# Kernel optimization log

Hardware: AMD Instinct MI355X
Metric: run time of the kernel (lower is better)

Reference implementation:

```python
import jax, jax.numpy as jnp
import numpy as np
from math import sqrt

N_HEADS = 16

def setup_inputs() -> dict:
    key = jax.random.key(0)
    ks = jax.random.split(key, 6)
    B, T, C = 4, 2048, 1024
    s = 0.02
    return {
        "X": jax.random.normal(ks[0], (B, T, C), jnp.float32),
        "Wq": jax.random.normal(ks[1], (C, C), jnp.float32) * s,
        "Wk": jax.random.normal(ks[2], (C, C), jnp.float32) * s,
        "Wv": jax.random.normal(ks[3], (C, C), jnp.float32) * s,
        "Wo": jax.random.normal(ks[4], (C, C), jnp.float32) * s,
        "bo": jnp.zeros((C,), jnp.float32),
    }

def reference(X, Wq, Wk, Wv, Wo, bo):
    B, T, C = X.shape
    H = N_HEADS
    D = C // H
    scale = sqrt(C / H)  # == sqrt(D)
    # Linear layers (torch Linear: y = x @ W.T), split into heads: [B,H,T,D]
    Q = (X @ Wq.T).reshape(B, T, H, D).transpose(0, 2, 1, 3)
    K = (X @ Wk.T).reshape(B, T, H, D).transpose(0, 2, 1, 3)
    V = (X @ Wv.T).reshape(B, T, H, D).transpose(0, 2, 1, 3)
    A = jnp.einsum("bhtd,bhsd->bhts", Q, K) / scale  # [B,H,T,T]
    causal = jnp.tril(jnp.ones((T, T), dtype=bool))
    A = jnp.where(causal, A, -jnp.inf)
    A = jax.nn.softmax(A, axis=-1)
    Y = jnp.einsum("bhts,bhsd->bhtd", A, V)  # [B,H,T,D]
    Y = Y.transpose(0, 2, 1, 3).reshape(B, T, C)
    return Y @ Wo.T + bo
```

## Files before the change

kernel.cpp:

```cpp
#include <hip/hip_runtime.h>
#include <hip/hip_bf16.h>
#include <stdint.h>


typedef unsigned short u16;
typedef __attribute__((ext_vector_type(8))) __bf16 bf16x8;
typedef __attribute__((ext_vector_type(4))) float  f32x4;
typedef __attribute__((ext_vector_type(4))) unsigned short u16x4;
typedef __attribute__((ext_vector_type(4))) short s16x4;

#define B_  4
#define T_  2048
#define C_  1024
#define H_  16
#define D_  64
#define BT_ (B_ * T_)

#define Q_SCALE 0.1803368801111204f

__device__ __forceinline__ u16 f32_to_bf16(float f) {
    unsigned int u = __float_as_uint(f);
    unsigned int r = (u + 0x7FFFu + ((u >> 16) & 1u)) >> 16;
    return (u16)r;
}

__device__ __forceinline__ unsigned int pk_bf16(float a, float b) {
    float2 f2; f2.x = a; f2.y = b;
    __hip_bfloat162 h = __float22bfloat162_rn(f2);
    return *(unsigned int*)&h;
}

__device__ __forceinline__ void async16(const void* g, void* lds) {
    __builtin_amdgcn_global_load_lds(
        (const __attribute__((address_space(1))) void*)g,
        (__attribute__((address_space(3))) void*)lds, 16, 0, 0);
}

__global__ void cast_bf16_kernel(const float* __restrict__ in, u16* __restrict__ out, int n4) {
    int i = blockIdx.x * 256 + threadIdx.x;
    if (i >= n4) return;
    float4 v = ((const float4*)in)[i];
    u16x4 o;
    o[0] = f32_to_bf16(v.x); o[1] = f32_to_bf16(v.y);
    o[2] = f32_to_bf16(v.z); o[3] = f32_to_bf16(v.w);
    ((u16x4*)out)[i] = o;
}

__global__ void cast_w4_kernel(const float* __restrict__ w0, const float* __restrict__ w1,
                               const float* __restrict__ w2, const float* __restrict__ w3,
                               u16* __restrict__ o0, u16* __restrict__ o1,
                               u16* __restrict__ o2, u16* __restrict__ o3) {
    int which = blockIdx.y;
    const float* in = (which == 0) ? w0 : (which == 1) ? w1 : (which == 2) ? w2 : w3;
    u16* out = (which == 0) ? o0 : (which == 1) ? o1 : (which == 2) ? o2 : o3;
    int i = blockIdx.x * 256 + threadIdx.x;
    float4 v = ((const float4*)in)[i];
    u16x4 o;
    o[0] = f32_to_bf16(v.x); o[1] = f32_to_bf16(v.y);
    o[2] = f32_to_bf16(v.z); o[3] = f32_to_bf16(v.w);
    ((u16x4*)out)[i] = o;
}

__device__ __forceinline__ void gemm_core_128_db(
    const u16* __restrict__ A, const u16* __restrict__ B,
    u16* As, u16* Bs, int m0, int n0, f32x4 (&acc)[4][4])
{
    const int K = C_;
    const int KT = K / 32;
    int tid  = threadIdx.x;
    int lane = tid & 63, w = tid >> 6;
    int quad = lane >> 4, l15 = lane & 15;
    int wm = w >> 1, wn = w & 1;

    int c0 = tid, c1 = tid + 256;
    int row0 = c0 >> 2, row1 = c1 >> 2;
    int gc0 = (((c0 & 3) - (row0 >> 1)) & 3) * 8;
    int gc1 = (((c1 & 3) - (row1 >> 1)) & 3) * 8;
    int ldsb0 = (w * 64) * 16;
    int ldsb1 = (256 + w * 64) * 16;

    const u16* ApA = A + (size_t)(m0 + row0) * K + gc0;
    const u16* ApB = A + (size_t)(m0 + row1) * K + gc1;
    const u16* BpA = B + (size_t)(n0 + row0) * K + gc0;
    const u16* BpB = B + (size_t)(n0 + row1) * K + gc1;

    char* As0 = (char*)As; char* As1 = (char*)As + 8192;
    char* Bs0 = (char*)Bs; char* Bs1 = (char*)Bs + 8192;

    int aoff[4], boff[4];
#pragma unroll
    for (int i = 0; i < 4; ++i) {
        int rA = wm * 64 + i * 16 + l15;
        aoff[i] = (rA * 32 + (((rA >> 1) + quad) & 3) * 8) * 2;
        int rB = wn * 64 + i * 16 + l15;
        boff[i] = (rB * 32 + (((rB >> 1) + quad) & 3) * 8) * 2;
    }

    async16(ApA, As0 + ldsb0); async16(ApB, As0 + ldsb1);
    async16(BpA, Bs0 + ldsb0); async16(BpB, Bs0 + ldsb1);
    ApA += 32; ApB += 32; BpA += 32; BpB += 32;

    auto body = [&](int kt, const char* Ac, const char* Bc, char* Apf, char* Bpf) {
        __syncthreads();
        if (kt + 1 < KT) {
            async16(ApA, Apf + ldsb0); async16(ApB, Apf + ldsb1);
            async16(BpA, Bpf + ldsb0); async16(BpB, Bpf + ldsb1);
        }
        ApA += 32; ApB += 32; BpA += 32; BpB += 32;

        bf16x8 a[4], b[4];
#pragma unroll
        for (int i = 0; i < 4; ++i) {
            a[i] = *(const bf16x8*)(Ac + aoff[i]);
            b[i] = *(const bf16x8*)(Bc + boff[i]);
        }
#pragma unroll
        for (int i = 0; i < 4; ++i)
#pragma unroll
            for (int j = 0; j < 4; ++j)
                acc[i][j] = __builtin_amdgcn_mfma_f32_16x16x32_bf16(a[i], b[j], acc[i][j], 0, 0, 0);
    };

    for (int kt = 0; kt < KT; kt += 2) {
        body(kt,     As0, Bs0, As1, Bs1);
        body(kt + 1, As1, Bs1, As0, Bs0);
    }
}

__global__ __launch_bounds__(256, 4) void qkv_gemm(
    const u16* __restrict__ Xb,
    const u16* __restrict__ Wqb, const u16* __restrict__ Wkb, const u16* __restrict__ Wvb,
    u16* __restrict__ Qb, u16* __restrict__ Kb, u16* __restrict__ Vtb)
{
    __shared__ u16 As[2 * 128 * 32];
    __shared__ u16 Bs[2 * 128 * 32];

    int id = blockIdx.x;
    int xcd = id & 7;
    int local = id >> 3;
    int yloc = local & 7;
    int zx = local >> 3;
    int bx = zx & 7;
    int which = zx >> 3;
    int by = xcd * 8 + yloc;

    const u16* W = (which == 0) ? Wqb : ((which == 1) ? Wkb : Wvb);

    f32x4 acc[4][4];
    const f32x4 z4 = {0.f, 0.f, 0.f, 0.f};
#pragma unroll
    for (int i = 0; i < 4; ++i)
#pragma unroll
        for (int j = 0; j < 4; ++j) acc[i][j] = z4;

    int lane = threadIdx.x & 63, w = threadIdx.x >> 6;
    int quad = lane >> 4, l15 = lane & 15;
    int wm = w >> 1, wn = w & 1;

    if (which <= 1) {
        int m0 = bx * 128, n0 = by * 128;
        gemm_core_128_db(W, Xb, As, Bs, m0, n0, acc);
        float s = (which == 0) ? Q_SCALE : 1.0f;
        u16* Out = (which == 0) ? Qb : Kb;
#pragma unroll
        for (int i = 0; i < 4; ++i) {
            int ch0 = m0 + wm * 64 + i * 16 + quad * 4;
#pragma unroll
            for (int j = 0; j < 4; ++j) {
                int t = n0 + wn * 64 + j * 16 + l15;
                u16x4 v;
#pragma unroll
                for (int r = 0; r < 4; ++r) v[r] = f32_to_bf16(acc[i][j][r] * s);
                *(u16x4*)&Out[(size_t)t * C_ + ch0] = v;
            }
        }
    } else {
        int m0 = by * 128, n0 = bx * 128;
        gemm_core_128_db(Xb, W, As, Bs, m0, n0, acc);
#pragma unroll
        for (int i = 0; i < 4; ++i) {
            int t0 = m0 + wm * 64 + i * 16 + quad * 4;
#pragma unroll
            for (int j = 0; j < 4; ++j) {
                int col = n0 + wn * 64 + j * 16 + l15;
                int h = col >> 6, d = col & 63;
                u16x4 v;
#pragma unroll
                for (int r = 0; r < 4; ++r) v[r] = f32_to_bf16(acc[i][j][r]);
                int b = t0 >> 11, t = t0 & (T_ - 1);
                *(u16x4*)&Vtb[(((b * H_ + h) * D_ + d) * T_) + t] = v;
            }
        }
    }
}

__global__ __launch_bounds__(256) void attn_kernel(
    const u16* __restrict__ Qb, const u16* __restrict__ Kb,
    const u16* __restrict__ Vtb, u16* __restrict__ Yb)
{
    __shared__ u16 Ks0[64 * 64], Ks1[64 * 64];
    __shared__ u16 Vs0[64 * 64], Vs1[64 * 64];

    int id = blockIdx.x;
    int kk = id >> 8;
    int cc = id & 255;
    int jj = cc >> 6;
    int bh = cc & 63;
    int qt = (kk == 0) ? jj : (kk == 1) ? (15 - jj) : (kk == 2) ? (jj + 4) : (11 - jj);

    int tid = threadIdx.x, lane = tid & 63, w = tid >> 6;
    int quad = lane >> 4, l15 = lane & 15;
    int qbase = qt * 128;
    int b = bh >> 4, h = bh & 15;

    bf16x8 qf[2][2];
    {
        const u16* q0 = Qb + ((size_t)(b * T_ + qbase + w * 32 + l15)) * C_ + h * 64;
        qf[0][0] = *(const bf16x8*)(q0 + quad * 8);
        qf[0][1] = *(const bf16x8*)(q0 + 32 + quad * 8);
        const u16* q1 = q0 + 16 * C_;
        qf[1][0] = *(const bf16x8*)(q1 + quad * 8);
        qf[1][1] = *(const bf16x8*)(q1 + 32 + quad * 8);
    }

    int koff0[4], koff1[4], voff[4][4];
#pragma unroll
    for (int sblk = 0; sblk < 4; ++sblk) {
        int sr = sblk * 16 + l15;
        koff0[sblk] = (sr * 64 + ((quad + sr) & 7) * 8) * 2;
        koff1[sblk] = (sr * 64 + ((4 + quad + sr) & 7) * 8) * 2;
    }
#pragma unroll
    for (int n = 0; n < 4; ++n)
#pragma unroll
        for (int sblk = 0; sblk < 4; ++sblk) {
            int dr = n * 16 + l15;
            voff[n][sblk] = (dr * 64 + ((sblk * 2 + (quad >> 1) + dr) & 7) * 8 + (quad & 1) * 4) * 2;
        }

    float l_part[2] = {0.f, 0.f};
    f32x4 o_acc[2][4];
    const f32x4 z4 = {0.f, 0.f, 0.f, 0.f};
#pragma unroll
    for (int c = 0; c < 2; ++c)
#pragma unroll
        for (int n = 0; n < 4; ++n) o_acc[c][n] = z4;

    int cA = tid, cB = tid + 256;
    int sA = cA >> 3, sB = cB >> 3;
    int offA = (((cA & 7) - sA) & 7) * 8;
    int offB = (((cB & 7) - sB) & 7) * 8;
    const u16* Kbase = Kb + (size_t)(b * T_) * C_ + h * 64;
    const u16* Vbase = Vtb + (size_t)bh * D_ * T_;
    int ldsb0 = (w * 64) * 16, ldsb1 = (256 + w * 64) * 16;

    const int nst = 2 * qt + 2;

    const u16* kgpA = Kbase + (size_t)sA * C_ + offA;
    const u16* kgpB = Kbase + (size_t)sB * C_ + offB;
    const u16* vgpA = Vbase + sA * T_ + offA;
    const u16* vgpB = Vbase + sB * T_ + offB;

    async16(kgpA, (char*)Ks0 + ldsb0);
    async16(kgpB, (char*)Ks0 + ldsb1);
    async16(vgpA, (char*)Vs0 + ldsb0);
    async16(vgpB, (char*)Vs0 + ldsb1);
    kgpA += 64 * C_; kgpB += 64 * C_; vgpA += 64; vgpB += 64;

    auto tile_body = [&](int st, const u16* K_, const u16* V_, char* Kpf, char* Vpf) {
        __syncthreads();
        if (st + 1 < nst) {
            async16(kgpA, Kpf + ldsb0);
            async16(kgpB, Kpf + ldsb1);
            async16(vgpA, Vpf + ldsb0);
            async16(vgpB, Vpf + ldsb1);
        }
        kgpA += 64 * C_; kgpB += 64 * C_; vgpA += 64; vgpB += 64;

        f32x4 sv[2][4];
#pragma unroll
        for (int sblk = 0; sblk < 4; ++sblk) {
            bf16x8 k0 = *(const bf16x8*)((const char*)K_ + koff0[sblk]);
            bf16x8 k1 = *(const bf16x8*)((const char*)K_ + koff1[sblk]);
#pragma unroll
            for (int c = 0; c < 2; ++c) {
                f32x4 t0 = __builtin_amdgcn_mfma_f32_16x16x32_bf16(k0, qf[c][0], z4, 0, 0, 0);
                sv[c][sblk] = __builtin_amdgcn_mfma_f32_16x16x32_bf16(k1, qf[c][1], t0, 0, 0, 0);
            }
        }

        if (st >= 2 * qt) {
            int sb0 = st * 64 - qbase;
#pragma unroll
            for (int c = 0; c < 2; ++c) {
                int tl = w * 32 + c * 16 + l15;
#pragma unroll
                for (int sblk = 0; sblk < 4; ++sblk)
#pragma unroll
                    for (int r = 0; r < 4; ++r)
                        if (sb0 + sblk * 16 + quad * 4 + r > tl) sv[c][sblk][r] = -1e30f;
            }
        }

        s16x4 pfrag[2][4];
#pragma unroll
        for (int c = 0; c < 2; ++c) {
            f32x4 s4 = z4;
#pragma unroll
            for (int sblk = 0; sblk < 4; ++sblk) {
#pragma unroll
                for (int r = 0; r < 4; ++r)
                    sv[c][sblk][r] = __builtin_amdgcn_exp2f(sv[c][sblk][r]);
                s4 += sv[c][sblk];
                uint2 pk;
                pk.x = pk_bf16(sv[c][sblk][0], sv[c][sblk][1]);
                pk.y = pk_bf16(sv[c][sblk][2], sv[c][sblk][3]);
                pfrag[c][sblk] = *(s16x4*)&pk;
            }
            l_part[c] += (s4[0] + s4[1]) + (s4[2] + s4[3]);
        }

#pragma unroll
        for (int n = 0; n < 4; ++n)
#pragma unroll
            for (int sblk = 0; sblk < 4; ++sblk) {
                s16x4 va = *(const s16x4*)((const char*)V_ + voff[n][sblk]);
#pragma unroll
                for (int c = 0; c < 2; ++c)
                    o_acc[c][n] = __builtin_amdgcn_mfma_f32_16x16x16bf16_1k(va, pfrag[c][sblk], o_acc[c][n], 0, 0, 0);
            }
    };

    for (int st = 0; st < nst; st += 2) {
        tile_body(st,     Ks0, Vs0, (char*)Ks1, (char*)Vs1);
        tile_body(st + 1, Ks1, Vs1, (char*)Ks0, (char*)Vs0);
    }

#pragma unroll
    for (int c = 0; c < 2; ++c) {
        float l = l_part[c];
        l += __shfl_xor(l, 16, 64);
        l += __shfl_xor(l, 32, 64);
        float inv = 1.0f / l;
        int t = qbase + w * 32 + c * 16 + l15;
        size_t rowoff = ((size_t)b * T_ + t) * C_ + h * 64;
#pragma unroll
        for (int n = 0; n < 4; ++n) {
            uint2 pk;
            pk.x = pk_bf16(o_acc[c][n][0] * inv, o_acc[c][n][1] * inv);
            pk.y = pk_bf16(o_acc[c][n][2] * inv, o_acc[c][n][3] * inv);
            *(uint2*)&Yb[rowoff + n * 16 + quad * 4] = pk;
        }
    }
}

__global__ __launch_bounds__(256, 4) void proj_gemm(
    const u16* __restrict__ Yb, const u16* __restrict__ Wob,
    const float* __restrict__ bo, float* __restrict__ out)
{
    __shared__ u16 As[2 * 128 * 32];
    __shared__ u16 Bs[2 * 128 * 32];

    int id = blockIdx.x;
    int xcd = id & 7;
    int local = id >> 3;
    int by = xcd * 8 + (local & 7);
    int bx = local >> 3;
    int m0 = bx * 128, n0 = by * 128;

    f32x4 acc[4][4];
    const f32x4 z4 = {0.f, 0.f, 0.f, 0.f};
#pragma unroll
    for (int i = 0; i < 4; ++i)
#pragma unroll
        for (int j = 0; j < 4; ++j) acc[i][j] = z4;

    gemm_core_128_db(Wob, Yb, As, Bs, m0, n0, acc);

    int lane = threadIdx.x & 63, w = threadIdx.x >> 6;
    int quad = lane >> 4, l15 = lane & 15;
    int wm = w >> 1, wn = w & 1;

#pragma unroll
    for (int i = 0; i < 4; ++i) {
        int ch0 = m0 + wm * 64 + i * 16 + quad * 4;
        float4 b4 = *(const float4*)&bo[ch0];
#pragma unroll
        for (int j = 0; j < 4; ++j) {
            int t = n0 + wn * 64 + j * 16 + l15;
            float4 o;
            o.x = acc[i][j][0] + b4.x;
            o.y = acc[i][j][1] + b4.y;
            o.z = acc[i][j][2] + b4.z;
            o.w = acc[i][j][3] + b4.w;
            *(float4*)&out[(size_t)t * C_ + ch0] = o;
        }
    }
}

extern "C" void kernel_launch(void* const* d_in, const int* in_sizes, int n_in,
                              void* d_out, int out_size, void* d_ws, size_t ws_size,
                              hipStream_t stream) {
    const float* X  = (const float*)d_in[0];
    const float* Wq = (const float*)d_in[1];
    const float* Wk = (const float*)d_in[2];
    const float* Wv = (const float*)d_in[3];
    const float* Wo = (const float*)d_in[4];
    const float* bo = (const float*)d_in[5];

    char* ws = (char*)d_ws;
    u16* Xb  = (u16*)(ws);
    u16* Wqb = (u16*)(ws + (16u << 20));
    u16* Wkb = (u16*)(ws + (18u << 20));
    u16* Wvb = (u16*)(ws + (20u << 20));
    u16* Wob = (u16*)(ws + (22u << 20));
    u16* Qb  = (u16*)(ws + (24u << 20));
    u16* Kb  = (u16*)(ws + (40u << 20));
    u16* Vtb = (u16*)(ws + (56u << 20));
    u16* Yb  = (u16*)(ws + (72u << 20));

    cast_bf16_kernel<<<(BT_ * C_ / 4) / 256, 256, 0, stream>>>(X, Xb, BT_ * C_ / 4);
    cast_w4_kernel<<<dim3((C_ * C_ / 4) / 256, 4), 256, 0, stream>>>(
        Wq, Wk, Wv, Wo, Wqb, Wkb, Wvb, Wob);

    qkv_gemm<<<dim3(3 * 8 * 64), 256, 0, stream>>>(Xb, Wqb, Wkb, Wvb, Qb, Kb, Vtb);
    attn_kernel<<<dim3((T_ / 128) * B_ * H_), 256, 0, stream>>>(Qb, Kb, Vtb, Yb);
    proj_gemm<<<dim3(8 * 64), 256, 0, stream>>>(Yb, Wob, bo, (float*)d_out);
}
```

Before: 278.8 us.

## Stage GEMM and attention epilogues through LDS for coalesced global stores

Epilogues of the QKV GEMM, attention and output projection now write accumulator fragments into padded shared memory and then read them back row-wise, so each global store is contiguous along the fast dimension. The old stores were strided 8- or 16-byte writes scattered across rows, which wasted memory transactions. The cost is extra LDS traffic and barriers, a slightly larger shared-memory footprint (17408 elements) that may affect occupancy, and for the projection two passes of staging with extra syncs.

```diff
diff --git a/kernel.cpp b/kernel.cpp
--- a/kernel.cpp
+++ b/kernel.cpp
@@ -7,6 +7,7 @@
 typedef __attribute__((ext_vector_type(8))) __bf16 bf16x8;
 typedef __attribute__((ext_vector_type(4))) float  f32x4;
 typedef __attribute__((ext_vector_type(4))) unsigned short u16x4;
+typedef __attribute__((ext_vector_type(8))) unsigned short u16x8;
 typedef __attribute__((ext_vector_type(4))) short s16x4;
 
 #define B_  4
@@ -132,8 +133,9 @@
     const u16* __restrict__ Wqb, const u16* __restrict__ Wkb, const u16* __restrict__ Wvb,
     u16* __restrict__ Qb, u16* __restrict__ Kb, u16* __restrict__ Vtb)
 {
-    __shared__ u16 As[2 * 128 * 32];
-    __shared__ u16 Bs[2 * 128 * 32];
+    __shared__ u16 SM[17408];
+    u16* As = SM;
+    u16* Bs = SM + 8192;
 
     int id = blockIdx.x;
     int xcd = id & 7;
@@ -153,7 +155,8 @@
 #pragma unroll
         for (int j = 0; j < 4; ++j) acc[i][j] = z4;
 
-    int lane = threadIdx.x & 63, w = threadIdx.x >> 6;
+    int tid = threadIdx.x;
+    int lane = tid & 63, w = tid >> 6;
     int quad = lane >> 4, l15 = lane & 15;
     int wm = w >> 1, wn = w & 1;
 
@@ -162,34 +165,56 @@
         gemm_core_128_db(W, Xb, As, Bs, m0, n0, acc);
         float s = (which == 0) ? Q_SCALE : 1.0f;
         u16* Out = (which == 0) ? Qb : Kb;
+
+        __syncthreads();
 #pragma unroll
         for (int i = 0; i < 4; ++i) {
-            int ch0 = m0 + wm * 64 + i * 16 + quad * 4;
+            int chl = wm * 64 + i * 16 + quad * 4;
 #pragma unroll
             for (int j = 0; j < 4; ++j) {
-                int t = n0 + wn * 64 + j * 16 + l15;
+                int tl = wn * 64 + j * 16 + l15;
                 u16x4 v;
 #pragma unroll
                 for (int r = 0; r < 4; ++r) v[r] = f32_to_bf16(acc[i][j][r] * s);
-                *(u16x4*)&Out[(size_t)t * C_ + ch0] = v;
-            }
+                *(u16x4*)&SM[tl * 132 + chl] = v;
+            }
+        }
+        __syncthreads();
+#pragma unroll
+        for (int st = 0; st < 16; ++st) {
+            int tl = w * 32 + st * 2 + (lane >> 5);
+            int ch4 = (lane & 31) * 4;
+            u16x4 v = *(u16x4*)&SM[tl * 132 + ch4];
+            *(u16x4*)&Out[(size_t)(n0 + tl) * C_ + m0 + ch4] = v;
         }
     } else {
         int m0 = by * 128, n0 = bx * 128;
         gemm_core_128_db(Xb, W, As, Bs, m0, n0, acc);
+
+        __syncthreads();
 #pragma unroll
         for (int i = 0; i < 4; ++i) {
-            int t0 = m0 + wm * 64 + i * 16 + quad * 4;
+            int tl0 = wm * 64 + i * 16 + quad * 4;
 #pragma unroll
             for (int j = 0; j < 4; ++j) {
-                int col = n0 + wn * 64 + j * 16 + l15;
-                int h = col >> 6, d = col & 63;
+                int chl = wn * 64 + j * 16 + l15;
                 u16x4 v;
 #pragma unroll
                 for (int r = 0; r < 4; ++r) v[r] = f32_to_bf16(acc[i][j][r]);
-                int b = t0 >> 11, t = t0 & (T_ - 1);
-                *(u16x4*)&Vtb[(((b * H_ + h) * D_ + d) * T_) + t] = v;
-            }
+                *(u16x4*)&SM[chl * 132 + tl0] = v;
+            }
+        }
+        __syncthreads();
+        int bb = m0 >> 11;
+        int tbase = m0 & (T_ - 1);
+#pragma unroll
+        for (int st = 0; st < 16; ++st) {
+            int chl = w * 32 + st * 2 + (lane >> 5);
+            int t4 = (lane & 31) * 4;
+            u16x4 v = *(u16x4*)&SM[chl * 132 + t4];
+            int col = n0 + chl;
+            int h = col >> 6, d = col & 63;
+            *(u16x4*)&Vtb[(((bb * H_ + h) * D_ + d) * T_) + tbase + t4] = v;
         }
     }
 }
@@ -198,8 +223,11 @@
     const u16* __restrict__ Qb, const u16* __restrict__ Kb,
     const u16* __restrict__ Vtb, u16* __restrict__ Yb)
 {
-    __shared__ u16 Ks0[64 * 64], Ks1[64 * 64];
-    __shared__ u16 Vs0[64 * 64], Vs1[64 * 64];
+    __shared__ u16 SMA[16384];
+    u16* Ks0 = SMA;
+    u16* Ks1 = SMA + 4096;
+    u16* Vs0 = SMA + 8192;
+    u16* Vs1 = SMA + 12288;
 
     int id = blockIdx.x;
     int kk = id >> 8;
@@ -336,21 +364,31 @@
         tile_body(st + 1, Ks1, Vs1, (char*)Ks0, (char*)Vs0);
     }
 
+    __syncthreads();
+    u16* PW = SMA + w * 2304;
 #pragma unroll
     for (int c = 0; c < 2; ++c) {
         float l = l_part[c];
         l += __shfl_xor(l, 16, 64);
         l += __shfl_xor(l, 32, 64);
         float inv = 1.0f / l;
-        int t = qbase + w * 32 + c * 16 + l15;
-        size_t rowoff = ((size_t)b * T_ + t) * C_ + h * 64;
 #pragma unroll
         for (int n = 0; n < 4; ++n) {
+            u16x4 v;
             uint2 pk;
             pk.x = pk_bf16(o_acc[c][n][0] * inv, o_acc[c][n][1] * inv);
             pk.y = pk_bf16(o_acc[c][n][2] * inv, o_acc[c][n][3] * inv);
-            *(uint2*)&Yb[rowoff + n * 16 + quad * 4] = pk;
-        }
+            v = *(u16x4*)&pk;
+            *(u16x4*)&PW[(c * 16 + l15) * 72 + n * 16 + quad * 4] = v;
+        }
+    }
+    asm volatile("s_waitcnt lgkmcnt(0)" ::: "memory");
+#pragma unroll
+    for (int st = 0; st < 4; ++st) {
+        int tr = st * 8 + (lane >> 3);
+        int d8 = (lane & 7) * 8;
+        u16x8 v = *(u16x8*)&PW[tr * 72 + d8];
+        *(u16x8*)&Yb[(size_t)(b * T_ + qbase + w * 32 + tr) * C_ + h * 64 + d8] = v;
     }
 }
 
@@ -358,8 +396,9 @@
     const u16* __restrict__ Yb, const u16* __restrict__ Wob,
     const float* __restrict__ bo, float* __restrict__ out)
 {
-    __shared__ u16 As[2 * 128 * 32];
-    __shared__ u16 Bs[2 * 128 * 32];
+    __shared__ u16 SM[17408];
+    u16* As = SM;
+    u16* Bs = SM + 8192;
 
     int id = blockIdx.x;
     int xcd = id & 7;
@@ -381,20 +420,32 @@
     int quad = lane >> 4, l15 = lane & 15;
     int wm = w >> 1, wn = w & 1;
 
-#pragma unroll
-    for (int i = 0; i < 4; ++i) {
-        int ch0 = m0 + wm * 64 + i * 16 + quad * 4;
-        float4 b4 = *(const float4*)&bo[ch0];
-#pragma unroll
-        for (int j = 0; j < 4; ++j) {
-            int t = n0 + wn * 64 + j * 16 + l15;
-            float4 o;
-            o.x = acc[i][j][0] + b4.x;
-            o.y = acc[i][j][1] + b4.y;
-            o.z = acc[i][j][2] + b4.z;
-            o.w = acc[i][j][3] + b4.w;
-            *(float4*)&out[(size_t)t * C_ + ch0] = o;
-        }
+    float* LF = (float*)SM;
+    __syncthreads();
+#pragma unroll
+    for (int hh = 0; hh < 2; ++hh) {
+        if (wm == hh) {
+#pragma unroll
+            for (int i = 0; i < 4; ++i) {
+                int chl = i * 16 + quad * 4;
+#pragma unroll
+                for (int j = 0; j < 4; ++j) {
+                    int tl = wn * 64 + j * 16 + l15;
+                    *(f32x4*)&LF[tl * 68 + chl] = acc[i][j];
+                }
+            }
+        }
+        __syncthreads();
+        f32x4 b4 = *(const f32x4*)&bo[m0 + hh * 64 + (lane & 15) * 4];
+#pragma unroll
+        for (int st = 0; st < 8; ++st) {
+            int tl = w * 32 + st * 4 + (lane >> 4);
+            int ch4 = (lane & 15) * 4;
+            f32x4 v = *(f32x4*)&LF[tl * 68 + ch4];
+            v += b4;
+            *(f32x4*)&out[(size_t)(n0 + tl) * C_ + m0 + hh * 64 + ch4] = v;
+        }
+        if (hh == 0) __syncthreads();
     }
 }
 
```

Result: slower. 285.7 us (+2.4%).
